# Kernel tuning notes

Hardware: AMD Instinct MI355X
Metric: run time of the kernel (lower is better)

## Reference

```python
import jax, jax.numpy as jnp
import numpy as np

B, T, C = 4, 2048, 1024
H, HS = 16, 64  # n_heads, head_size; H*HS == C


def setup_inputs() -> dict:
    key = jax.random.key(0)
    ks = jax.random.split(key, 6)
    s = 0.02
    x = jax.random.normal(ks[0], (B, T, C), dtype=jnp.float32)
    Wq = jax.random.normal(ks[1], (H, C, HS), dtype=jnp.float32) * s
    Wk = jax.random.normal(ks[2], (H, C, HS), dtype=jnp.float32) * s
    Wv = jax.random.normal(ks[3], (H, C, HS), dtype=jnp.float32) * s
    Wo = jax.random.normal(ks[4], (C, C), dtype=jnp.float32) * s
    bo = jnp.zeros((C,), dtype=jnp.float32)
    return {"x": x, "Wq": Wq, "Wk": Wk, "Wv": Wv, "Wo": Wo, "bo": bo}


def reference(x, Wq, Wk, Wv, Wo, bo):
    # batched multi-head causal attention (math identical to per-head loop)
    q = jnp.einsum('btc,hcd->bhtd', x, Wq)  # [B,H,T,HS]
    k = jnp.einsum('btc,hcd->bhtd', x, Wk)
    v = jnp.einsum('btc,hcd->bhtd', x, Wv)
    scale = 1.0 / jnp.sqrt(jnp.asarray(HS, x.dtype))
    scores = jnp.einsum('bhtd,bhsd->bhts', q, k) * scale  # [B,H,T,T]
    causal = jnp.tril(jnp.ones((T, T), dtype=bool))
    scores = jnp.where(causal, scores, jnp.asarray(-jnp.inf, scores.dtype))
    attn = jax.nn.softmax(scores, axis=-1)
    out = jnp.einsum('bhts,bhsd->bhtd', attn, v)  # [B,H,T,HS]
    # concat heads along feature dim (head order == module list order)
    out = out.transpose(0, 2, 1, 3).reshape(B, T, C)
    return out @ Wo.T + bo
```

## Files before the change

### kernel.cpp

```cpp
#include <hip/hip_runtime.h>

typedef __attribute__((ext_vector_type(8))) short v8s;
typedef __attribute__((ext_vector_type(4))) short v4s;
typedef __attribute__((ext_vector_type(4))) float v4f;

static __device__ __forceinline__ short f2bf(float f) {
  union { float f; unsigned u; } c; c.f = f;
  unsigned r = c.u + 0x7fffu + ((c.u >> 16) & 1u);
  return (short)(r >> 16);
}

static __device__ __forceinline__ unsigned pk_bf16(float a, float b) {
  union { float f; unsigned u; } ca, cb; ca.f = a; cb.f = b;
  return ((ca.u + 0x8000u) >> 16) | ((cb.u + 0x8000u) & 0xffff0000u);
}

#define GLDS(gp, lp) __builtin_amdgcn_global_load_lds( \
    (const __attribute__((address_space(1))) void*)(gp), \
    (__attribute__((address_space(3))) void*)(lp), 16, 0, 0)


__global__ __launch_bounds__(256) void cast_f32_bf16(const float* __restrict__ src,
                                                     short* __restrict__ dst) {
  int idx = (blockIdx.x * 256 + threadIdx.x) * 4;
  float4 v = *(const float4*)(src + idx);
  v4s o; o.x = f2bf(v.x); o.y = f2bf(v.y); o.z = f2bf(v.z); o.w = f2bf(v.w);
  *(v4s*)(dst + idx) = o;
}

__global__ __launch_bounds__(256) void build_wt(const float* __restrict__ Wq,
                                                const float* __restrict__ Wk,
                                                const float* __restrict__ Wv,
                                                short* __restrict__ Wt) {
  __shared__ float tile[64][65];
  int blk = blockIdx.x;
  int sel = blk >> 8, rest = blk & 255;
  int h = rest >> 4, kt = rest & 15;
  const float* W = (sel == 0) ? Wq : ((sel == 1) ? Wk : Wv);
  int k0 = kt * 64;
  int tid = threadIdx.x;
  for (int i = 0; i < 4; ++i) {
    int c = i * 256 + tid;
    int row = c >> 4, c4 = (c & 15) * 4;
    float4 v = *(const float4*)(W + (size_t)h * 65536 + (size_t)(k0 + row) * 64 + c4);
    tile[row][c4 + 0] = v.x; tile[row][c4 + 1] = v.y;
    tile[row][c4 + 2] = v.z; tile[row][c4 + 3] = v.w;
  }
  __syncthreads();
  for (int i = 0; i < 2; ++i) {
    int c = i * 256 + tid;
    int d = c >> 3, k8 = (c & 7) * 8;
    v8s o;
    for (int j = 0; j < 8; ++j) o[j] = f2bf(tile[k8 + j][d]);
    *(v8s*)(Wt + (size_t)(sel * 1024 + h * 64 + d) * 1024 + k0 + k8) = o;
  }
}

__global__ __launch_bounds__(256) void transpose_v(const short* __restrict__ V,
                                                   short* __restrict__ Vt) {
  __shared__ short tile[64][72];
  int bh = blockIdx.x >> 5, tt = blockIdx.x & 31;
  int t0 = tt * 64;
  int tid = threadIdx.x;
  for (int i = 0; i < 2; ++i) {
    int c = i * 256 + tid;
    int row = c >> 3, col8 = (c & 7) * 8;
    v8s v = *(const v8s*)(V + ((size_t)(bh * 2048 + t0 + row)) * 64 + col8);
    *(v8s*)&tile[row][col8] = v;
  }
  __syncthreads();
  for (int i = 0; i < 2; ++i) {
    int c = i * 256 + tid;
    int d = c >> 3, t8 = (c & 7) * 8;
    v8s o;
    for (int j = 0; j < 8; ++j) o[j] = tile[t8 + j][d];
    *(v8s*)(Vt + ((size_t)(bh * 64 + d)) * 2048 + t0 + t8) = o;
  }
}


__global__ __launch_bounds__(256) void gemm_qkv(const short* __restrict__ Xb,
                                                const short* __restrict__ Wt,
                                                short* __restrict__ Qo,
                                                short* __restrict__ Ko,
                                                short* __restrict__ Vo) {
  __shared__ short lA[128 * 32];
  __shared__ short lB[128 * 32];
  const int tid = threadIdx.x;
  const int lane = tid & 63, quad = lane >> 4, l16 = lane & 15;
  const int wave = tid >> 6;
  const int m0 = blockIdx.x * 128, n0 = blockIdx.y * 128;
  const int wm = (wave >> 1) * 64, wn = (wave & 1) * 64;
  v4f acc[4][4];
  for (int i = 0; i < 4; ++i)
    for (int j = 0; j < 4; ++j) acc[i][j] = (v4f){0.f, 0.f, 0.f, 0.f};

  for (int k0 = 0; k0 < 1024; k0 += 32) {
    __syncthreads();
    for (int i = 0; i < 2; ++i) {
      int c = i * 256 + tid;
      int row = c >> 2, kc = c & 3;
      GLDS(Xb + (size_t)(m0 + row) * 1024 + k0 + kc * 8, lA + c * 8);
      GLDS(Wt + (size_t)(n0 + row) * 1024 + k0 + kc * 8, lB + c * 8);
    }
    __syncthreads();
    v8s a[4], b[4];
    for (int mt = 0; mt < 4; ++mt) a[mt] = *(const v8s*)&lA[(wm + mt * 16 + l16) * 32 + quad * 8];
    for (int nt = 0; nt < 4; ++nt) b[nt] = *(const v8s*)&lB[(wn + nt * 16 + l16) * 32 + quad * 8];
    for (int mt = 0; mt < 4; ++mt)
      for (int nt = 0; nt < 4; ++nt)
        acc[mt][nt] = __builtin_amdgcn_mfma_f32_16x16x32_bf16(a[mt], b[nt], acc[mt][nt], 0, 0, 0);
  }

  int selu = n0 >> 10;
  short* obase = (selu == 0) ? Qo : ((selu == 1) ? Ko : Vo);
  for (int nt = 0; nt < 4; ++nt) {
    int n = n0 + wn + nt * 16 + l16;
    int hd = n & 1023;
    int h = hd >> 6, d = hd & 63;
    for (int mt = 0; mt < 4; ++mt)
      for (int r = 0; r < 4; ++r) {
        int m = m0 + wm + mt * 16 + quad * 4 + r;
        int b_ = m >> 11, t = m & 2047;
        obase[(size_t)((b_ * 16 + h) * 2048 + t) * 64 + d] = f2bf(acc[mt][nt][r]);
      }
  }
}


__global__ __launch_bounds__(256) void attn(const short* __restrict__ Q,
                                            const short* __restrict__ K,
                                            const short* __restrict__ Vt,
                                            short* __restrict__ AO) {
  __shared__ short lK[64 * 64];
  __shared__ short lV[64 * 64];
  __shared__ short lP[4 * 16 * 72];
  const int tid = threadIdx.x;
  const int w = tid >> 6, lane = tid & 63, quad = lane >> 4, l16 = lane & 15;
  const int bh = blockIdx.x & 63, pr = blockIdx.x >> 6;
  const float kexp = 0.18033688011112042f;
  const unsigned psel = 0x07060302u;
  short* pw = lP + w * (16 * 72);
  const size_t qkbase = (size_t)bh * 2048 * 64;
  const size_t vtbase = (size_t)bh * 64 * 2048;
  const int b_ = bh >> 4, h = bh & 15;

  const int r0 = tid >> 3, cp = tid & 7;
  const int cl0 = cp ^ (r0 & 7);
  const int r1 = r0 + 32;
  const int cl1 = cp ^ (r1 & 7);

  const int swz = l16 & 7;
  const int ph0 = (quad ^ swz) * 8;
  const int ph1 = ((quad + 4) ^ swz) * 8;

  for (int phase = 0; phase < 2; ++phase) {
    const int c = phase ? (31 - pr) : pr;
    const int q0 = c * 64 + w * 16;

    v8s bQ0, bQ1;
    {
      const short* qb = Q + qkbase + (size_t)(q0 + l16) * 64 + quad * 8;
      bQ0 = *(const v8s*)(qb);
      bQ1 = *(const v8s*)(qb + 32);
    }
    v4f accO[4];
    for (int g = 0; g < 4; ++g) accO[g] = (v4f){0.f, 0.f, 0.f, 0.f};
    float lrun = 0.f;

    for (int kt = 0; kt <= c; ++kt) {
      const int kb = kt * 64;
      __syncthreads();
      GLDS(K + qkbase + (size_t)(kb + r0) * 64 + cl0 * 8, lK + tid * 8);
      GLDS(K + qkbase + (size_t)(kb + r1) * 64 + cl1 * 8, lK + tid * 8 + 2048);
      GLDS(Vt + vtbase + (size_t)r0 * 2048 + kb + cl0 * 8, lV + tid * 8);
      GLDS(Vt + vtbase + (size_t)r1 * 2048 + kb + cl1 * 8, lV + tid * 8 + 2048);
      __syncthreads();

      v4f sT[4];
#pragma unroll
      for (int mt = 0; mt < 4; ++mt) {
        const short* kr = lK + (mt * 16 + l16) * 64;
        v8s aK0 = *(const v8s*)(kr + ph0);
        v8s aK1 = *(const v8s*)(kr + ph1);
        v4f t = (v4f){0.f, 0.f, 0.f, 0.f};
        t = __builtin_amdgcn_mfma_f32_16x16x32_bf16(aK0, bQ0, t, 0, 0, 0);
        t = __builtin_amdgcn_mfma_f32_16x16x32_bf16(aK1, bQ1, t, 0, 0, 0);
        sT[mt] = t;
      }
      if (kt == c) {
        const int kq = kb + quad * 4 - (q0 + l16);
#pragma unroll
        for (int mt = 0; mt < 4; ++mt)
#pragma unroll
          for (int r = 0; r < 4; ++r)
            if (kq + mt * 16 + r > 0) sT[mt][r] = -__builtin_inff();
      }
#pragma unroll
      for (int mt = 0; mt < 4; ++mt) {
        float p0 = exp2f(sT[mt][0] * kexp);
        float p1 = exp2f(sT[mt][1] * kexp);
        float p2 = exp2f(sT[mt][2] * kexp);
        float p3 = exp2f(sT[mt][3] * kexp);
        lrun += (p0 + p1) + (p2 + p3);
        int2 dw;
        dw.x = (int)__builtin_amdgcn_perm(__float_as_uint(p1), __float_as_uint(p0), psel);
        dw.y = (int)__builtin_amdgcn_perm(__float_as_uint(p3), __float_as_uint(p2), psel);
        *(int2*)&pw[l16 * 72 + mt * 16 + quad * 4] = dw;
      }
      v8s bP0 = *(const v8s*)&pw[l16 * 72 + quad * 8];
      v8s bP1 = *(const v8s*)&pw[l16 * 72 + 32 + quad * 8];
#pragma unroll
      for (int g = 0; g < 4; ++g) {
        const short* vr = lV + (g * 16 + l16) * 64;
        v8s aV0 = *(const v8s*)(vr + ph0);
        v8s aV1 = *(const v8s*)(vr + ph1);
        accO[g] = __builtin_amdgcn_mfma_f32_16x16x32_bf16(aV0, bP0, accO[g], 0, 0, 0);
        accO[g] = __builtin_amdgcn_mfma_f32_16x16x32_bf16(aV1, bP1, accO[g], 0, 0, 0);
      }
    }

    lrun += __shfl_xor(lrun, 16);
    lrun += __shfl_xor(lrun, 32);
    float inv = __builtin_amdgcn_rcpf(lrun);
    int t = q0 + l16;
    short* ao = AO + ((size_t)(b_ * 2048 + t)) * 1024 + h * 64 + quad * 4;
#pragma unroll
    for (int g = 0; g < 4; ++g) {
      int2 dw;
      dw.x = (int)pk_bf16(accO[g][0] * inv, accO[g][1] * inv);
      dw.y = (int)pk_bf16(accO[g][2] * inv, accO[g][3] * inv);
      *(int2*)(ao + g * 16) = dw;
    }
  }
}


__global__ __launch_bounds__(256) void gemm_out(const short* __restrict__ AO,
                                                const short* __restrict__ Wot,
                                                const float* __restrict__ bo,
                                                float* __restrict__ out) {
  __shared__ short lA[128 * 32];
  __shared__ short lB[128 * 32];
  const int tid = threadIdx.x;
  const int lane = tid & 63, quad = lane >> 4, l16 = lane & 15;
  const int wave = tid >> 6;
  const int m0 = blockIdx.x * 128, n0 = blockIdx.y * 128;
  const int wm = (wave >> 1) * 64, wn = (wave & 1) * 64;
  v4f acc[4][4];
  for (int i = 0; i < 4; ++i)
    for (int j = 0; j < 4; ++j) acc[i][j] = (v4f){0.f, 0.f, 0.f, 0.f};

  for (int k0 = 0; k0 < 1024; k0 += 32) {
    __syncthreads();
    for (int i = 0; i < 2; ++i) {
      int c = i * 256 + tid;
      int row = c >> 2, kc = c & 3;
      GLDS(AO + (size_t)(m0 + row) * 1024 + k0 + kc * 8, lA + c * 8);
      GLDS(Wot + (size_t)(n0 + row) * 1024 + k0 + kc * 8, lB + c * 8);
    }
    __syncthreads();
    v8s a[4], b[4];
    for (int mt = 0; mt < 4; ++mt) a[mt] = *(const v8s*)&lA[(wm + mt * 16 + l16) * 32 + quad * 8];
    for (int nt = 0; nt < 4; ++nt) b[nt] = *(const v8s*)&lB[(wn + nt * 16 + l16) * 32 + quad * 8];
    for (int mt = 0; mt < 4; ++mt)
      for (int nt = 0; nt < 4; ++nt)
        acc[mt][nt] = __builtin_amdgcn_mfma_f32_16x16x32_bf16(a[mt], b[nt], acc[mt][nt], 0, 0, 0);
  }

  for (int nt = 0; nt < 4; ++nt) {
    int n = n0 + wn + nt * 16 + l16;
    float bias = bo[n];
    for (int mt = 0; mt < 4; ++mt)
      for (int r = 0; r < 4; ++r) {
        int m = m0 + wm + mt * 16 + quad * 4 + r;
        out[(size_t)m * 1024 + n] = acc[mt][nt][r] + bias;
      }
  }
}


extern "C" void kernel_launch(void* const* d_in, const int* in_sizes, int n_in,
                              void* d_out, int out_size, void* d_ws, size_t ws_size,
                              hipStream_t stream) {
  const float* x  = (const float*)d_in[0];
  const float* Wq = (const float*)d_in[1];
  const float* Wk = (const float*)d_in[2];
  const float* Wv = (const float*)d_in[3];
  const float* Wo = (const float*)d_in[4];
  const float* bo = (const float*)d_in[5];
  float* out = (float*)d_out;
  char* ws = (char*)d_ws;

  short* Xb  = (short*)(ws);
  short* Wt  = (short*)(ws + (16u << 20));
  short* Wot = (short*)(ws + (22u << 20));
  short* Q   = (short*)(ws + (24u << 20));
  short* K   = (short*)(ws + (40u << 20));
  short* V   = (short*)(ws + (56u << 20));
  short* Vt  = (short*)(ws + (72u << 20));

  cast_f32_bf16<<<8192, 256, 0, stream>>>(x, Xb);
  cast_f32_bf16<<<1024, 256, 0, stream>>>(Wo, Wot);
  build_wt<<<768, 256, 0, stream>>>(Wq, Wk, Wv, Wt);
  gemm_qkv<<<dim3(64, 24), 256, 0, stream>>>(Xb, Wt, Q, K, V);
  transpose_v<<<2048, 256, 0, stream>>>(V, Vt);
  attn<<<dim3(1024), 256, 0, stream>>>(Q, K, Vt, Xb);
  gemm_out<<<dim3(64, 8), 256, 0, stream>>>(Xb, Wot, bo, out);
}
```

Measured before the change: 270.4 us.

## Enlarge attention query tile to 128 rows per block and reuse K/V tiles

Each block now handles 128 query rows, with 32 rows per wave split into two 16-row subtiles, instead of 64. Each K/V tile staged in LDS is reused for twice as many queries, and the grid is halved to 512 blocks. Causal masking is redone per subtile and fully masked subtiles are skipped. The change also swaps exp2f for the hardware exp2 builtin and adds a launch-bounds occupancy hint, in exchange for more registers, fewer blocks, and idle waves on diagonal tiles.

```diff
diff --git a/kernel.cpp b/kernel.cpp
--- a/kernel.cpp
+++ b/kernel.cpp
@@ -14,6 +14,12 @@
   union { float f; unsigned u; } ca, cb; ca.f = a; cb.f = b;
   return ((ca.u + 0x8000u) >> 16) | ((cb.u + 0x8000u) & 0xffff0000u);
 }
+
+#if __has_builtin(__builtin_amdgcn_exp2f)
+#define EXP2(x) __builtin_amdgcn_exp2f(x)
+#else
+#define EXP2(x) exp2f(x)
+#endif
 
 #define GLDS(gp, lp) __builtin_amdgcn_global_load_lds( \
     (const __attribute__((address_space(1))) void*)(gp), \
@@ -128,19 +134,19 @@
 }
 
 
-__global__ __launch_bounds__(256) void attn(const short* __restrict__ Q,
-                                            const short* __restrict__ K,
-                                            const short* __restrict__ Vt,
-                                            short* __restrict__ AO) {
+__global__ __launch_bounds__(256, 2) void attn(const short* __restrict__ Q,
+                                               const short* __restrict__ K,
+                                               const short* __restrict__ Vt,
+                                               short* __restrict__ AO) {
   __shared__ short lK[64 * 64];
   __shared__ short lV[64 * 64];
-  __shared__ short lP[4 * 16 * 72];
+  __shared__ short lP[4 * 32 * 72];
   const int tid = threadIdx.x;
   const int w = tid >> 6, lane = tid & 63, quad = lane >> 4, l16 = lane & 15;
   const int bh = blockIdx.x & 63, pr = blockIdx.x >> 6;
   const float kexp = 0.18033688011112042f;
   const unsigned psel = 0x07060302u;
-  short* pw = lP + w * (16 * 72);
+  short* pw = lP + w * (32 * 72);
   const size_t qkbase = (size_t)bh * 2048 * 64;
   const size_t vtbase = (size_t)bh * 64 * 2048;
   const int b_ = bh >> 4, h = bh & 15;
@@ -155,20 +161,24 @@
   const int ph1 = ((quad + 4) ^ swz) * 8;
 
   for (int phase = 0; phase < 2; ++phase) {
-    const int c = phase ? (31 - pr) : pr;
-    const int q0 = c * 64 + w * 16;
-
-    v8s bQ0, bQ1;
-    {
-      const short* qb = Q + qkbase + (size_t)(q0 + l16) * 64 + quad * 8;
-      bQ0 = *(const v8s*)(qb);
-      bQ1 = *(const v8s*)(qb + 32);
-    }
-    v4f accO[4];
-    for (int g = 0; g < 4; ++g) accO[g] = (v4f){0.f, 0.f, 0.f, 0.f};
-    float lrun = 0.f;
-
-    for (int kt = 0; kt <= c; ++kt) {
+    const int c = phase ? (15 - pr) : pr;
+    const int qc = c * 128 + w * 32;
+
+    v8s bQ[2][2];
+#pragma unroll
+    for (int qs = 0; qs < 2; ++qs) {
+      const short* qb = Q + qkbase + (size_t)(qc + qs * 16 + l16) * 64 + quad * 8;
+      bQ[qs][0] = *(const v8s*)(qb);
+      bQ[qs][1] = *(const v8s*)(qb + 32);
+    }
+    v4f accO[2][4];
+#pragma unroll
+    for (int qs = 0; qs < 2; ++qs)
+      for (int g = 0; g < 4; ++g) accO[qs][g] = (v4f){0.f, 0.f, 0.f, 0.f};
+    float lrun[2] = {0.f, 0.f};
+
+    const int nst = 2 * c + 2;
+    for (int kt = 0; kt < nst; ++kt) {
       const int kb = kt * 64;
       __syncthreads();
       GLDS(K + qkbase + (size_t)(kb + r0) * 64 + cl0 * 8, lK + tid * 8);
@@ -177,60 +187,87 @@
       GLDS(Vt + vtbase + (size_t)r1 * 2048 + kb + cl1 * 8, lV + tid * 8 + 2048);
       __syncthreads();
 
-      v4f sT[4];
+      const bool act0 = kb < qc + 16;
+      const bool act1 = kb < qc + 32;
+      if (!act1) continue;
+
+      v8s aK[4][2];
 #pragma unroll
       for (int mt = 0; mt < 4; ++mt) {
         const short* kr = lK + (mt * 16 + l16) * 64;
-        v8s aK0 = *(const v8s*)(kr + ph0);
-        v8s aK1 = *(const v8s*)(kr + ph1);
-        v4f t = (v4f){0.f, 0.f, 0.f, 0.f};
-        t = __builtin_amdgcn_mfma_f32_16x16x32_bf16(aK0, bQ0, t, 0, 0, 0);
-        t = __builtin_amdgcn_mfma_f32_16x16x32_bf16(aK1, bQ1, t, 0, 0, 0);
-        sT[mt] = t;
-      }
-      if (kt == c) {
-        const int kq = kb + quad * 4 - (q0 + l16);
-#pragma unroll
-        for (int mt = 0; mt < 4; ++mt)
-#pragma unroll
-          for (int r = 0; r < 4; ++r)
-            if (kq + mt * 16 + r > 0) sT[mt][r] = -__builtin_inff();
-      }
-#pragma unroll
-      for (int mt = 0; mt < 4; ++mt) {
-        float p0 = exp2f(sT[mt][0] * kexp);
-        float p1 = exp2f(sT[mt][1] * kexp);
-        float p2 = exp2f(sT[mt][2] * kexp);
-        float p3 = exp2f(sT[mt][3] * kexp);
-        lrun += (p0 + p1) + (p2 + p3);
-        int2 dw;
-        dw.x = (int)__builtin_amdgcn_perm(__float_as_uint(p1), __float_as_uint(p0), psel);
-        dw.y = (int)__builtin_amdgcn_perm(__float_as_uint(p3), __float_as_uint(p2), psel);
-        *(int2*)&pw[l16 * 72 + mt * 16 + quad * 4] = dw;
-      }
-      v8s bP0 = *(const v8s*)&pw[l16 * 72 + quad * 8];
-      v8s bP1 = *(const v8s*)&pw[l16 * 72 + 32 + quad * 8];
+        aK[mt][0] = *(const v8s*)(kr + ph0);
+        aK[mt][1] = *(const v8s*)(kr + ph1);
+      }
+#pragma unroll
+      for (int qs = 0; qs < 2; ++qs) {
+        if (qs == 0 ? !act0 : false) continue;
+        const int rbase = qc + qs * 16;
+        v4f sT[4];
+#pragma unroll
+        for (int mt = 0; mt < 4; ++mt) {
+          v4f t = (v4f){0.f, 0.f, 0.f, 0.f};
+          t = __builtin_amdgcn_mfma_f32_16x16x32_bf16(aK[mt][0], bQ[qs][0], t, 0, 0, 0);
+          t = __builtin_amdgcn_mfma_f32_16x16x32_bf16(aK[mt][1], bQ[qs][1], t, 0, 0, 0);
+          sT[mt] = t;
+        }
+        if (kb + 63 >= rbase) {
+          const int kq = kb + quad * 4 - (rbase + l16);
+#pragma unroll
+          for (int mt = 0; mt < 4; ++mt)
+#pragma unroll
+            for (int r = 0; r < 4; ++r)
+              if (kq + mt * 16 + r > 0) sT[mt][r] = -__builtin_inff();
+        }
+        float ls = lrun[qs];
+#pragma unroll
+        for (int mt = 0; mt < 4; ++mt) {
+          float p0 = EXP2(sT[mt][0] * kexp);
+          float p1 = EXP2(sT[mt][1] * kexp);
+          float p2 = EXP2(sT[mt][2] * kexp);
+          float p3 = EXP2(sT[mt][3] * kexp);
+          ls += (p0 + p1) + (p2 + p3);
+          int2 dw;
+          dw.x = (int)__builtin_amdgcn_perm(__float_as_uint(p1), __float_as_uint(p0), psel);
+          dw.y = (int)__builtin_amdgcn_perm(__float_as_uint(p3), __float_as_uint(p2), psel);
+          *(int2*)&pw[(qs * 16 + l16) * 72 + mt * 16 + quad * 4] = dw;
+        }
+        lrun[qs] = ls;
+      }
+      v8s aV[4][2];
 #pragma unroll
       for (int g = 0; g < 4; ++g) {
         const short* vr = lV + (g * 16 + l16) * 64;
-        v8s aV0 = *(const v8s*)(vr + ph0);
-        v8s aV1 = *(const v8s*)(vr + ph1);
-        accO[g] = __builtin_amdgcn_mfma_f32_16x16x32_bf16(aV0, bP0, accO[g], 0, 0, 0);
-        accO[g] = __builtin_amdgcn_mfma_f32_16x16x32_bf16(aV1, bP1, accO[g], 0, 0, 0);
-      }
-    }
-
-    lrun += __shfl_xor(lrun, 16);
-    lrun += __shfl_xor(lrun, 32);
-    float inv = __builtin_amdgcn_rcpf(lrun);
-    int t = q0 + l16;
-    short* ao = AO + ((size_t)(b_ * 2048 + t)) * 1024 + h * 64 + quad * 4;
-#pragma unroll
-    for (int g = 0; g < 4; ++g) {
-      int2 dw;
-      dw.x = (int)pk_bf16(accO[g][0] * inv, accO[g][1] * inv);
-      dw.y = (int)pk_bf16(accO[g][2] * inv, accO[g][3] * inv);
-      *(int2*)(ao + g * 16) = dw;
+        aV[g][0] = *(const v8s*)(vr + ph0);
+        aV[g][1] = *(const v8s*)(vr + ph1);
+      }
+#pragma unroll
+      for (int qs = 0; qs < 2; ++qs) {
+        if (qs == 0 ? !act0 : false) continue;
+        v8s bP0 = *(const v8s*)&pw[(qs * 16 + l16) * 72 + quad * 8];
+        v8s bP1 = *(const v8s*)&pw[(qs * 16 + l16) * 72 + 32 + quad * 8];
+#pragma unroll
+        for (int g = 0; g < 4; ++g) {
+          accO[qs][g] = __builtin_amdgcn_mfma_f32_16x16x32_bf16(aV[g][0], bP0, accO[qs][g], 0, 0, 0);
+          accO[qs][g] = __builtin_amdgcn_mfma_f32_16x16x32_bf16(aV[g][1], bP1, accO[qs][g], 0, 0, 0);
+        }
+      }
+    }
+
+#pragma unroll
+    for (int qs = 0; qs < 2; ++qs) {
+      float ls = lrun[qs];
+      ls += __shfl_xor(ls, 16);
+      ls += __shfl_xor(ls, 32);
+      float inv = __builtin_amdgcn_rcpf(ls);
+      int t = qc + qs * 16 + l16;
+      short* ao = AO + ((size_t)(b_ * 2048 + t)) * 1024 + h * 64 + quad * 4;
+#pragma unroll
+      for (int g = 0; g < 4; ++g) {
+        int2 dw;
+        dw.x = (int)pk_bf16(accO[qs][g][0] * inv, accO[qs][g][1] * inv);
+        dw.y = (int)pk_bf16(accO[qs][g][2] * inv, accO[qs][g][3] * inv);
+        *(int2*)(ao + g * 16) = dw;
+      }
     }
   }
 }
@@ -305,6 +342,6 @@
   build_wt<<<768, 256, 0, stream>>>(Wq, Wk, Wv, Wt);
   gemm_qkv<<<dim3(64, 24), 256, 0, stream>>>(Xb, Wt, Q, K, V);
   transpose_v<<<2048, 256, 0, stream>>>(V, Vt);
-  attn<<<dim3(1024), 256, 0, stream>>>(Q, K, Vt, Xb);
+  attn<<<dim3(512), 256, 0, stream>>>(Q, K, Vt, Xb);
   gemm_out<<<dim3(64, 8), 256, 0, stream>>>(Xb, Wot, bo, out);
 }
```

After: 247.9 us. 8.3% less time.
